# Optimization experiments

Hardware: AMD Instinct MI355X
Metric: run time of the kernel (lower is better)

The kernel has to match this reference:

```python
import jax, jax.numpy as jnp
import numpy as np

D_MODEL, D_K, D_V, N_HEADS = 1024, 64, 64, 16
B, S = 4, 4096
LN_EPS = 1e-5
NORM_EPS = 1e-12  # torch F.normalize default eps


def setup_inputs() -> dict:
    key = jax.random.key(0)
    ks = jax.random.split(key, 9)
    s = 0.02
    return {
        "x": jax.random.normal(ks[0], (B, S, D_MODEL), dtype=jnp.float32),
        # nn.Linear weights have shape [out, in]
        "W_Q": jax.random.normal(ks[1], (N_HEADS * D_K, D_MODEL), dtype=jnp.float32) * s,
        "W_K": jax.random.normal(ks[2], (N_HEADS * D_K, D_MODEL), dtype=jnp.float32) * s,
        "W_V": jax.random.normal(ks[3], (N_HEADS * D_V, D_MODEL), dtype=jnp.float32) * s,
        "W_g": jax.random.normal(ks[4], (N_HEADS * D_V, D_MODEL), dtype=jnp.float32) * s,
        "W_alpha": jax.random.normal(ks[5], (N_HEADS, D_MODEL), dtype=jnp.float32) * s,
        "W_O": jax.random.normal(ks[6], (D_MODEL, N_HEADS * D_V), dtype=jnp.float32) * s,
        "ln_gamma": jnp.ones((D_MODEL,), dtype=jnp.float32),
        "ln_beta": jnp.zeros((D_MODEL,), dtype=jnp.float32),
    }


def reference(x, W_Q, W_K, W_V, W_g, W_alpha, W_O, ln_gamma, ln_beta):
    # --- input projection chain (unfused variant) ---
    Q_raw = jnp.einsum('bsd,od->bso', x, W_Q)               # [B,S,H*Dk] (unused downstream)
    K_raw = jnp.einsum('bsd,od->bso', x, W_K)               # [B,S,H*Dk]
    V = jnp.einsum('bsd,od->bso', x, W_V)                   # [B,S,H*Dv]
    g_raw = jnp.einsum('bsd,od->bso', x, W_g)               # [B,S,H*Dv]
    alpha_raw = jnp.einsum('bsd,od->bso', x, W_alpha)       # [B,S,H]

    # F.normalize over the full last dim (n_heads*d_k), eps clamp on the norm
    K_norm = K_raw / jnp.maximum(jnp.linalg.norm(K_raw, axis=-1, keepdims=True), NORM_EPS)
    gate = jax.nn.silu(g_raw)
    alpha = jax.nn.sigmoid(alpha_raw)

    # scan is simulated as identity: scan_output = V
    scan_output = V

    # --- output epilogue: gate-multiply + output GEMM + residual + LayerNorm ---
    gated = scan_output * gate
    projected = jnp.einsum('bsv,dv->bsd', gated, W_O)
    pre = projected + x
    mean = jnp.mean(pre, axis=-1, keepdims=True)
    var = jnp.mean(jnp.square(pre - mean), axis=-1, keepdims=True)
    out = (pre - mean) * jax.lax.rsqrt(var + LN_EPS) * ln_gamma + ln_beta
    return out
```

## Files before the change

### kernel.cpp

```cpp
#include <hip/hip_runtime.h>

#define M_TOT 16384
#define DM    1024

typedef unsigned short ushort_t;
typedef __bf16 bf16x8 __attribute__((ext_vector_type(8)));
typedef float  f32x4  __attribute__((ext_vector_type(4)));

__device__ __forceinline__ ushort_t f32_to_bf16(float f) {
    union { float f; unsigned u; } v; v.f = f;
    unsigned u = v.u;
    return (ushort_t)((u + 0x7fffu + ((u >> 16) & 1u)) >> 16);
}
__device__ __forceinline__ float bf16_to_f32(ushort_t h) {
    union { unsigned u; float f; } v; v.u = ((unsigned)h) << 16;
    return v.f;
}

__device__ __forceinline__ void gload16(const ushort_t* g, ushort_t* l) {
    __builtin_amdgcn_global_load_lds(
        (const __attribute__((address_space(1))) unsigned int*)g,
        (__attribute__((address_space(3))) unsigned int*)l,
        16, 0, 0);
}

__global__ __launch_bounds__(256) void cvt_all(const float* __restrict__ x,
                                               const float* __restrict__ wv,
                                               const float* __restrict__ wg,
                                               const float* __restrict__ wo,
                                               ushort_t* __restrict__ xb,
                                               ushort_t* __restrict__ wcat,
                                               ushort_t* __restrict__ wob) {
    const long NX = (long)M_TOT * DM / 4, NW = (long)DM * DM / 4;
    long i = (long)blockIdx.x * 256 + threadIdx.x;
    const float* src; ushort_t* dst; long so, di;
    if (i < NX) {
        src = x; so = i; dst = xb; di = i;
    } else if (i < NX + NW) {
        long j = i - NX; src = wv; so = j;
        int row = (int)(j >> 8), c4 = (int)(j & 255);
        int orow = ((row >> 4) << 5) | (row & 15);
        dst = wcat; di = (long)orow * 256 + c4;
    } else if (i < NX + 2 * NW) {
        long j = i - NX - 2 * NW + NW;
        j = i - NX - NW; src = wg; so = j;
        int row = (int)(j >> 8), c4 = (int)(j & 255);
        int orow = ((row >> 4) << 5) | 16 | (row & 15);
        dst = wcat; di = (long)orow * 256 + c4;
    } else {
        long j = i - NX - 2 * NW; src = wo; so = j; dst = wob; di = j;
    }
    const float4 v = ((const float4*)src)[so];
    ushort4 o;
    o.x = f32_to_bf16(v.x); o.y = f32_to_bf16(v.y);
    o.z = f32_to_bf16(v.z); o.w = f32_to_bf16(v.w);
    ((ushort4*)dst)[di] = o;
}

template<int EPI>
__global__ __launch_bounds__(512, 2) void gemm8p(
    const ushort_t* __restrict__ A,
    const ushort_t* __restrict__ B,
    const ushort_t* __restrict__ Xb,
    ushort_t* __restrict__ out,
    int nchunk)
{
    extern __shared__ ushort_t lds[];

    const int flat = blockIdx.x;
    const int wgid = (flat & 7) * nchunk + (flat >> 3);
    const int m0 = (wgid & 63) << 8;
    const int n0 = (wgid >> 6) << 8;

    const int tid  = threadIdx.x;
    const int w    = tid >> 6;
    const int l    = tid & 63;
    const int wm   = w >> 2;
    const int wn   = w & 3;
    const int fr   = l & 15;
    const int quad = l >> 4;

    f32x4 acc[8][4];
    const f32x4 vzero = {0.f, 0.f, 0.f, 0.f};
#pragma unroll
    for (int i = 0; i < 8; ++i)
#pragma unroll
        for (int j = 0; j < 4; ++j) acc[i][j] = vzero;

    int srcA[2], srcB[2];
#pragma unroll
    for (int h = 0; h < 2; ++h) {
        srcA[h] = (m0 + h * 128 + w * 16 + fr) * DM + (quad << 3);
        srcB[h] = (n0 + h * 128 + w * 16 + fr) * DM + (quad << 3);
    }

    auto stage = [&](int u2) {
        const int cS   = u2 & 1;
        const int bufS = (u2 >> 1) & 1;
        const int koff = (u2 >> 1) * 64 + cS * 32;
        const int dA   = bufS * 16384 + (cS * 8 + w) * 512;
#pragma unroll
        for (int h = 0; h < 2; ++h) {
            gload16(A + srcA[h] + koff, lds + dA + h * 8192);
            gload16(B + srcB[h] + koff, lds + 32768 + dA + h * 8192);
        }
    };

    stage(0); stage(1);

    for (int u = 0; u < 32; ++u) {
        if (u < 30) {
            stage(u + 2);
            asm volatile("s_waitcnt vmcnt(8)" ::: "memory");
        } else if (u == 30) {
            asm volatile("s_waitcnt vmcnt(4)" ::: "memory");
        } else {
            asm volatile("s_waitcnt vmcnt(0)" ::: "memory");
        }
        __builtin_amdgcn_s_barrier();

        const int buf = (u >> 1) & 1, c = u & 1;
        const int abase = buf * 16384 + wm * 8192 + c * 4096 + l * 8;
        const int bbase = 32768 + buf * 16384 + (wn >> 1) * 8192
                        + (c * 8 + (wn & 1) * 4) * 512 + l * 8;
        bf16x8 bfrag[4], afrag[8];
#pragma unroll
        for (int j = 0; j < 4; ++j) bfrag[j] = *(const bf16x8*)(lds + bbase + j * 512);
#pragma unroll
        for (int i = 0; i < 8; ++i) afrag[i] = *(const bf16x8*)(lds + abase + i * 512);

        __builtin_amdgcn_s_setprio(1);
#pragma unroll
        for (int j = 0; j < 4; ++j)
#pragma unroll
            for (int i = 0; i < 8; ++i)
                acc[i][j] = __builtin_amdgcn_mfma_f32_16x16x32_bf16(
                    afrag[i], bfrag[j], acc[i][j], 0, 0, 0);
        __builtin_amdgcn_s_setprio(0);
    }

    const int rowb = m0 + wm * 128;
    const int colb = n0 + wn * 64;
    if (EPI == 0) {
#pragma unroll
        for (int i = 0; i < 8; ++i)
#pragma unroll
            for (int jp = 0; jp < 2; ++jp) {
                const int cb   = colb + jp * 32;
                const int vcol = ((cb >> 5) << 4) + fr;
#pragma unroll
                for (int r = 0; r < 4; ++r) {
                    const int row = rowb + i * 16 + quad * 4 + r;
                    float v = acc[i][2 * jp][r];
                    float g = acc[i][2 * jp + 1][r];
                    float gate = g / (1.0f + __expf(-g));
                    out[row * DM + vcol] = f32_to_bf16(v * gate);
                }
            }
    } else {
#pragma unroll
        for (int i = 0; i < 8; ++i)
#pragma unroll
            for (int j = 0; j < 4; ++j) {
                const int col = colb + j * 16 + fr;
#pragma unroll
                for (int r = 0; r < 4; ++r) {
                    const int row = rowb + i * 16 + quad * 4 + r;
                    float pre = acc[i][j][r] + bf16_to_f32(Xb[row * DM + col]);
                    out[row * DM + col] = f32_to_bf16(pre);
                }
            }
    }
}

__global__ __launch_bounds__(256) void ln_rows(const ushort_t* __restrict__ pre,
                                               const float* __restrict__ gamma,
                                               const float* __restrict__ beta,
                                               float* __restrict__ out)
{
    const int row = blockIdx.x;
    const int tid = threadIdx.x;
    const int wave = tid >> 6, lane = tid & 63;

    ushort4 u = ((const ushort4*)(pre + row * DM))[tid];
    float p0 = bf16_to_f32(u.x), p1 = bf16_to_f32(u.y);
    float p2 = bf16_to_f32(u.z), p3 = bf16_to_f32(u.w);

    float s  = p0 + p1 + p2 + p3;
    float ss = p0 * p0 + p1 * p1 + p2 * p2 + p3 * p3;
#pragma unroll
    for (int off = 32; off > 0; off >>= 1) {
        s  += __shfl_down(s, off);
        ss += __shfl_down(ss, off);
    }
    __shared__ float red[8];
    __shared__ float mb[2];
    if (lane == 0) { red[wave] = s; red[4 + wave] = ss; }
    __syncthreads();
    if (tid == 0) {
        float S  = red[0] + red[1] + red[2] + red[3];
        float SS = red[4] + red[5] + red[6] + red[7];
        float mean = S * (1.0f / 1024.0f);
        float var  = SS * (1.0f / 1024.0f) - mean * mean;
        mb[0] = mean;
        mb[1] = rsqrtf(var + 1e-5f);
    }
    __syncthreads();
    const float mean = mb[0], rs = mb[1];

    float4 gm = ((const float4*)gamma)[tid];
    float4 bt = ((const float4*)beta)[tid];
    float4 o;
    o.x = (p0 - mean) * rs * gm.x + bt.x;
    o.y = (p1 - mean) * rs * gm.y + bt.y;
    o.z = (p2 - mean) * rs * gm.z + bt.z;
    o.w = (p3 - mean) * rs * gm.w + bt.w;
    ((float4*)(out + row * DM))[tid] = o;
}

extern "C" void kernel_launch(void* const* d_in, const int* in_sizes, int n_in,
                              void* d_out, int out_size, void* d_ws, size_t ws_size,
                              hipStream_t stream) {
    const float* x     = (const float*)d_in[0];
    const float* WV    = (const float*)d_in[3];
    const float* WG    = (const float*)d_in[4];
    const float* WO    = (const float*)d_in[6];
    const float* gamma = (const float*)d_in[7];
    const float* beta  = (const float*)d_in[8];
    float* out = (float*)d_out;

    char* ws = (char*)d_ws;
    ushort_t* xb    = (ushort_t*)ws;
    ushort_t* gated = (ushort_t*)(ws + (size_t)M_TOT * DM * 2);
    ushort_t* wcat  = (ushort_t*)(ws + (size_t)M_TOT * DM * 4);
    ushort_t* wob   = (ushort_t*)(ws + (size_t)M_TOT * DM * 4 + (size_t)2 * DM * DM * 2);
    ushort_t* pre   = xb;

    static bool attr_set = false;
    if (!attr_set) {
        hipFuncSetAttribute((const void*)&gemm8p<0>,
                            hipFuncAttributeMaxDynamicSharedMemorySize, 131072);
        hipFuncSetAttribute((const void*)&gemm8p<1>,
                            hipFuncAttributeMaxDynamicSharedMemorySize, 131072);
        attr_set = true;
    }

    const int nCvt = (M_TOT * DM + 3 * DM * DM) / 4 / 256;
    cvt_all<<<nCvt, 256, 0, stream>>>(x, WV, WG, WO, xb, wcat, wob);

    gemm8p<0><<<512, 512, 131072, stream>>>(xb, wcat, nullptr, gated, 64);
    gemm8p<1><<<256, 512, 131072, stream>>>(gated, wob, xb, pre, 32);

    ln_rows<<<M_TOT, 256, 0, stream>>>(pre, gamma, beta, out);
}
```

Before: 273.9 us.

## Restructure GEMM mainloop into 4-stage ring with split A/B staging and 8-wave ping-pong

Replaces the two-buffer, two-chunk LDS staging with a 4-slot ring buffer of 32-wide K slices. A and B loads are issued separately between two half-MFMA phases separated by barriers, so the waves alternate between loading and computing. The workgroup-to-tile mapping also changes so that each XCD covers a contiguous block of M rows across all N tiles, aiming at better L2 reuse. The added barriers raise synchronisation cost, and the LDS layout has changed, which risks correctness errors.

```diff
diff --git a/kernel.cpp b/kernel.cpp
--- a/kernel.cpp
+++ b/kernel.cpp
@@ -42,8 +42,7 @@
         int orow = ((row >> 4) << 5) | (row & 15);
         dst = wcat; di = (long)orow * 256 + c4;
     } else if (i < NX + 2 * NW) {
-        long j = i - NX - 2 * NW + NW;
-        j = i - NX - NW; src = wg; so = j;
+        long j = i - NX - NW; src = wg; so = j;
         int row = (int)(j >> 8), c4 = (int)(j & 255);
         int orow = ((row >> 4) << 5) | 16 | (row & 15);
         dst = wcat; di = (long)orow * 256 + c4;
@@ -63,14 +62,15 @@
     const ushort_t* __restrict__ B,
     const ushort_t* __restrict__ Xb,
     ushort_t* __restrict__ out,
-    int nchunk)
+    int nbs)
 {
     extern __shared__ ushort_t lds[];
 
     const int flat = blockIdx.x;
-    const int wgid = (flat & 7) * nchunk + (flat >> 3);
-    const int m0 = (wgid & 63) << 8;
-    const int n0 = (wgid >> 6) << 8;
+    const int xcd  = flat & 7;
+    const int ii   = flat >> 3;
+    const int m0   = ((xcd << 3) + (ii >> nbs)) << 8;
+    const int n0   = (ii & ((1 << nbs) - 1)) << 8;
 
     const int tid  = threadIdx.x;
     const int w    = tid >> 6;
@@ -87,56 +87,73 @@
 #pragma unroll
         for (int j = 0; j < 4; ++j) acc[i][j] = vzero;
 
-    int srcA[2], srcB[2];
-#pragma unroll
-    for (int h = 0; h < 2; ++h) {
-        srcA[h] = (m0 + h * 128 + w * 16 + fr) * DM + (quad << 3);
-        srcB[h] = (n0 + h * 128 + w * 16 + fr) * DM + (quad << 3);
-    }
-
-    auto stage = [&](int u2) {
-        const int cS   = u2 & 1;
-        const int bufS = (u2 >> 1) & 1;
-        const int koff = (u2 >> 1) * 64 + cS * 32;
-        const int dA   = bufS * 16384 + (cS * 8 + w) * 512;
-#pragma unroll
-        for (int h = 0; h < 2; ++h) {
-            gload16(A + srcA[h] + koff, lds + dA + h * 8192);
-            gload16(B + srcB[h] + koff, lds + 32768 + dA + h * 8192);
-        }
+    const int sA0 = (m0 + w * 16 + fr) * DM + (quad << 3);
+    const int sA1 = sA0 + 128 * DM;
+    const int sB0 = (n0 + w * 16 + fr) * DM + (quad << 3);
+    const int sB1 = sB0 + 128 * DM;
+
+    auto stageA = [&](int u) {
+        const int d  = (u & 3) * 8192 + w * 512;
+        const int ko = u * 32;
+        gload16(A + sA0 + ko, lds + d);
+        gload16(A + sA1 + ko, lds + d + 4096);
     };
-
-    stage(0); stage(1);
+    auto stageB = [&](int u) {
+        const int d  = 32768 + (u & 3) * 8192 + w * 512;
+        const int ko = u * 32;
+        gload16(B + sB0 + ko, lds + d);
+        gload16(B + sB1 + ko, lds + d + 4096);
+    };
+
+    const int rA = wm * 4096 + l * 8;
+    const int rB = 32768 + wn * 2048 + l * 8;
+
+    stageA(0); stageB(0);
+    stageA(1); stageB(1);
+    stageA(2); stageB(2);
+    asm volatile("s_waitcnt vmcnt(8)" ::: "memory");
+    __builtin_amdgcn_s_barrier();
 
     for (int u = 0; u < 32; ++u) {
-        if (u < 30) {
-            stage(u + 2);
-            asm volatile("s_waitcnt vmcnt(8)" ::: "memory");
-        } else if (u == 30) {
-            asm volatile("s_waitcnt vmcnt(4)" ::: "memory");
-        } else {
-            asm volatile("s_waitcnt vmcnt(0)" ::: "memory");
-        }
-        __builtin_amdgcn_s_barrier();
-
-        const int buf = (u >> 1) & 1, c = u & 1;
-        const int abase = buf * 16384 + wm * 8192 + c * 4096 + l * 8;
-        const int bbase = 32768 + buf * 16384 + (wn >> 1) * 8192
-                        + (c * 8 + (wn & 1) * 4) * 512 + l * 8;
-        bf16x8 bfrag[4], afrag[8];
-#pragma unroll
-        for (int j = 0; j < 4; ++j) bfrag[j] = *(const bf16x8*)(lds + bbase + j * 512);
-#pragma unroll
-        for (int i = 0; i < 8; ++i) afrag[i] = *(const bf16x8*)(lds + abase + i * 512);
-
+        const int sb = (u & 3) * 8192;
+        bf16x8 bf[4], af[4];
+
+#pragma unroll
+        for (int j = 0; j < 4; ++j) bf[j] = *(const bf16x8*)(lds + sb + rB + j * 512);
+#pragma unroll
+        for (int i = 0; i < 4; ++i) af[i] = *(const bf16x8*)(lds + sb + rA + i * 512);
+        if (u < 29) stageA(u + 3);
+        __builtin_amdgcn_sched_barrier(0);
+        __builtin_amdgcn_s_barrier();
         __builtin_amdgcn_s_setprio(1);
 #pragma unroll
         for (int j = 0; j < 4; ++j)
 #pragma unroll
-            for (int i = 0; i < 8; ++i)
+            for (int i = 0; i < 4; ++i)
                 acc[i][j] = __builtin_amdgcn_mfma_f32_16x16x32_bf16(
-                    afrag[i], bfrag[j], acc[i][j], 0, 0, 0);
+                    af[i], bf[j], acc[i][j], 0, 0, 0);
         __builtin_amdgcn_s_setprio(0);
+        __builtin_amdgcn_sched_barrier(0);
+        __builtin_amdgcn_s_barrier();
+
+#pragma unroll
+        for (int i = 0; i < 4; ++i) af[i] = *(const bf16x8*)(lds + sb + rA + (4 + i) * 512);
+        if (u < 29) stageB(u + 3);
+        if (u < 29)       { asm volatile("s_waitcnt vmcnt(8)" ::: "memory"); }
+        else if (u == 29) { asm volatile("s_waitcnt vmcnt(4)" ::: "memory"); }
+        else if (u == 30) { asm volatile("s_waitcnt vmcnt(0)" ::: "memory"); }
+        __builtin_amdgcn_sched_barrier(0);
+        __builtin_amdgcn_s_barrier();
+        __builtin_amdgcn_s_setprio(1);
+#pragma unroll
+        for (int j = 0; j < 4; ++j)
+#pragma unroll
+            for (int i = 0; i < 4; ++i)
+                acc[4 + i][j] = __builtin_amdgcn_mfma_f32_16x16x32_bf16(
+                    af[i], bf[j], acc[4 + i][j], 0, 0, 0);
+        __builtin_amdgcn_s_setprio(0);
+        __builtin_amdgcn_sched_barrier(0);
+        __builtin_amdgcn_s_barrier();
     }
 
     const int rowb = m0 + wm * 128;
@@ -248,8 +265,8 @@
     const int nCvt = (M_TOT * DM + 3 * DM * DM) / 4 / 256;
     cvt_all<<<nCvt, 256, 0, stream>>>(x, WV, WG, WO, xb, wcat, wob);
 
-    gemm8p<0><<<512, 512, 131072, stream>>>(xb, wcat, nullptr, gated, 64);
-    gemm8p<1><<<256, 512, 131072, stream>>>(gated, wob, xb, pre, 32);
+    gemm8p<0><<<512, 512, 131072, stream>>>(xb, wcat, nullptr, gated, 3);
+    gemm8p<1><<<256, 512, 131072, stream>>>(gated, wob, xb, pre, 2);
 
     ln_rows<<<M_TOT, 256, 0, stream>>>(pre, gamma, beta, out);
 }
```

Result: no change. 274.5 us (+0.2%).
